# Kernel optimization log

Measured on AMD Instinct MI355X. Metric: run time of the kernel, lower is better.

## Reference

```python
import jax, jax.numpy as jnp
import numpy as np

DIM = 1024
NH = 16
HD = DIM // NH  # 64
NT = max(1, int(NH * 0.25))  # 4 time heads
NS = NH - NT                 # 12 space heads
SCALE = HD ** (-0.5)


def setup_inputs() -> dict:
    key = jax.random.key(0)
    ks = jax.random.split(key, 8)
    B, T = 2, 2048
    init = 0.02
    return {
        "x": jax.random.normal(ks[0], (B, T, DIM), dtype=jnp.float32),
        # weights stored as (in, out); torch Linear y = x @ W.T is equivalent
        "Wqt": jax.random.normal(ks[1], (DIM, NT * HD), dtype=jnp.float32) * init,
        "Wkt": jax.random.normal(ks[2], (DIM, NT * HD), dtype=jnp.float32) * init,
        "Wqs": jax.random.normal(ks[3], (DIM, NS * HD), dtype=jnp.float32) * init,
        "Wks": jax.random.normal(ks[4], (DIM, NS * HD), dtype=jnp.float32) * init,
        "Wv": jax.random.normal(ks[5], (DIM, DIM), dtype=jnp.float32) * init,
        "Wout": jax.random.normal(ks[6], (DIM, DIM), dtype=jnp.float32) * init,
        "bout": jnp.zeros((DIM,), dtype=jnp.float32),
        "w_sigma": jnp.zeros((1,), dtype=jnp.float32),
    }


def reference(x, Wqt, Wkt, Wqs, Wks, Wv, Wout, bout, w_sigma):
    B, T, D = x.shape
    Qt = (x @ Wqt).reshape(B, T, NT, HD)
    Kt = (x @ Wkt).reshape(B, T, NT, HD)
    Qs = (x @ Wqs).reshape(B, T, NS, HD)
    Ks = (x @ Wks).reshape(B, T, NS, HD)
    st = jnp.einsum('bthd,bshd->bths', Qt, Kt)  # [B,T,NT,T]
    ss = jnp.einsum('bthd,bshd->bths', Qs, Ks)  # [B,T,NS,T]
    sig = jax.nn.sigmoid(w_sigma)  # shape (1,), broadcasts
    score = jnp.concatenate([-sig * st, ss], axis=2) * SCALE  # [B,T,NH,T]
    attn = jax.nn.softmax(score, axis=-1)
    V = (x @ Wv).reshape(B, T, NH, HD)
    ctx = jnp.einsum('bths,bshd->bthd', attn, V).reshape(B, T, D)
    return ctx @ Wout + bout
```

## Files before the change

### kernel.cpp

```cpp
#include <hip/hip_runtime.h>
#include <hip/hip_bf16.h>

typedef __bf16 bf16_t;
typedef __bf16 bf16x2 __attribute__((ext_vector_type(2)));
typedef __bf16 bf16x4 __attribute__((ext_vector_type(4)));
typedef __bf16 bf16x8 __attribute__((ext_vector_type(8)));
typedef float  f32x4  __attribute__((ext_vector_type(4)));

#define DIM     1024
#define NHEAD   16
#define HDIM    64
#define NTIME   4
#define TSEQ    2048
#define NBATCH  2
#define SCALE_F 0.125f
#define LOG2E   1.4426950408889634f

#define GLL(gp, lp) __builtin_amdgcn_global_load_lds( \
    (const __attribute__((address_space(1))) unsigned int*)(const void*)(gp), \
    (__attribute__((address_space(3))) unsigned int*)(void*)(lp), 16, 0, 0)

#define OFF_WQKVT 0UL
#define OFF_WOUTT (OFF_WQKVT + 3072UL*1024UL*2UL)
#define OFF_Q     (OFF_WOUTT + 1024UL*1024UL*2UL)
#define OFF_K     (OFF_Q  + 2UL*16UL*2048UL*64UL*2UL)
#define OFF_VT    (OFF_K  + 2UL*16UL*2048UL*64UL*2UL)
#define OFF_CTX   (OFF_VT + 2UL*16UL*2048UL*64UL*2UL)

__global__ void prep_all(const float* __restrict__ x,
                         const float* __restrict__ Wqt, const float* __restrict__ Wkt,
                         const float* __restrict__ Wqs, const float* __restrict__ Wks,
                         const float* __restrict__ Wv,  const float* __restrict__ Wout,
                         bf16_t* __restrict__ Xb, bf16_t* __restrict__ WqkvT,
                         bf16_t* __restrict__ WoutT) {
    __shared__ float T[64][65];
    const int bid = blockIdx.x;
    if (bid < 2048) {
        int i = bid * 256 + threadIdx.x;
        const float4* s = (const float4*)(x + (size_t)i * 8);
        float4 a = s[0], b2 = s[1];
        bf16x8 v;
        v[0] = (bf16_t)a.x;  v[1] = (bf16_t)a.y;  v[2] = (bf16_t)a.z;  v[3] = (bf16_t)a.w;
        v[4] = (bf16_t)b2.x; v[5] = (bf16_t)b2.y; v[6] = (bf16_t)b2.z; v[7] = (bf16_t)b2.w;
        *(bf16x8*)(Xb + (size_t)i * 8) = v;
        return;
    }
    const int tc = threadIdx.x & 63, tr = threadIdx.x >> 6;
    const int sc = threadIdx.x & 31, sr = threadIdx.x >> 5;
    if (bid < 2816) {
        const int l = bid - 2048;
        const int n0 = (l % 48) * 64;
        const int k0 = (l / 48) * 64;
        const int region = n0 >> 10;
        const int cc = n0 & 1023;
        const int h = cc >> 6;
        const float* src; int ncols, col0;
        if (region == 2) { src = Wv; ncols = 1024; col0 = cc; }
        else if (h < NTIME) { src = (region == 0) ? Wqt : Wkt; ncols = NTIME * HDIM; col0 = h * HDIM; }
        else                { src = (region == 0) ? Wqs : Wks; ncols = (NHEAD - NTIME) * HDIM; col0 = (h - NTIME) * HDIM; }
#pragma unroll
        for (int i = 0; i < 16; ++i) {
            int kl = tr * 16 + i;
            T[kl][tc] = src[(size_t)(k0 + kl) * ncols + col0 + tc];
        }
        __syncthreads();
#pragma unroll
        for (int i = 0; i < 8; ++i) {
            int nl = sr * 8 + i;
            bf16x2 w;
            w[0] = (bf16_t)T[sc * 2][nl];
            w[1] = (bf16_t)T[sc * 2 + 1][nl];
            *(bf16x2*)(WqkvT + (size_t)(n0 + nl) * 1024 + k0 + sc * 2) = w;
        }
    } else {
        const int l = bid - 2816;
        const int n0 = (l % 16) * 64;
        const int k0 = (l / 16) * 64;
#pragma unroll
        for (int i = 0; i < 16; ++i) {
            int kl = tr * 16 + i;
            T[kl][tc] = Wout[(size_t)(k0 + kl) * 1024 + n0 + tc];
        }
        __syncthreads();
#pragma unroll
        for (int i = 0; i < 8; ++i) {
            int nl = sr * 8 + i;
            bf16x2 w;
            w[0] = (bf16_t)T[sc * 2][nl];
            w[1] = (bf16_t)T[sc * 2 + 1][nl];
            *(bf16x2*)(WoutT + (size_t)(n0 + nl) * 1024 + k0 + sc * 2) = w;
        }
    }
}

template<int MODE, int NB, int FN>
__global__ __launch_bounds__(256)
void gemm_bf16(const bf16_t* __restrict__ Ab, const bf16_t* __restrict__ Bt,
               bf16_t* __restrict__ Qb, bf16_t* __restrict__ Kb, bf16_t* __restrict__ Vt,
               float* __restrict__ Cout, const float* __restrict__ bias)
{
    __shared__ __align__(16) bf16_t As[3][128][32];
    __shared__ __align__(16) bf16_t Bs[3][FN * 32][32];

    constexpr int NXC = NB / 8;
    const int xcd = blockIdx.x & 7;
    const int r   = blockIdx.x >> 3;
    const int m0 = (r / NXC) * 128;
    const int n0 = (xcd * NXC + r % NXC) * (FN * 32);

    const int tid  = threadIdx.x;
    const int lane = tid & 63;
    const int wave = tid >> 6;
    const int wm = (wave >> 1) * 64, wn = (wave & 1) * (FN * 16);
    const int g = lane >> 4, lr = lane & 15;

    f32x4 acc[4][FN];
#pragma unroll
    for (int i = 0; i < 4; ++i)
#pragma unroll
        for (int j = 0; j < FN; ++j) acc[i][j] = f32x4{0.f, 0.f, 0.f, 0.f};

    auto stage = [&](int k0, int buf) {
#pragma unroll
        for (int c = 0; c < 2; ++c) {
            int idx  = tid + c * 256;
            int row  = idx >> 2;
            int csrc = (idx & 3) ^ ((row >> 1) & 3);
            GLL(Ab + (size_t)(m0 + row) * 1024 + k0 + csrc * 8,
                (char*)&As[buf][0][0] + (c * 256 + wave * 64) * 16);
            if (c < FN / 2)
                GLL(Bt + (size_t)(n0 + row) * 1024 + k0 + csrc * 8,
                    (char*)&Bs[buf][0][0] + (c * 256 + wave * 64) * 16);
        }
    };

    stage(0, 0);
    stage(32, 1);

    for (int t = 0; t < 32; ++t) {
        if (t < 31) {
            if constexpr (FN == 4) asm volatile("s_waitcnt vmcnt(4)" ::: "memory");
            else                   asm volatile("s_waitcnt vmcnt(3)" ::: "memory");
        } else {
            asm volatile("s_waitcnt vmcnt(0)" ::: "memory");
        }
        __builtin_amdgcn_s_barrier();
        __builtin_amdgcn_sched_barrier(0);
        if (t + 2 < 32) stage((t + 2) * 32, (t + 2) % 3);

        const int buf = t % 3;
        const char* Ac = (const char*)&As[buf][0][0];
        const char* Bc = (const char*)&Bs[buf][0][0];
        bf16x8 afr[4], bfr[FN];
#pragma unroll
        for (int f = 0; f < 4; ++f) {
            int ra = wm + f * 16 + lr;
            afr[f] = *(const bf16x8*)(Ac + ra * 64 + ((g ^ ((ra >> 1) & 3)) << 4));
        }
#pragma unroll
        for (int f = 0; f < FN; ++f) {
            int rb = wn + f * 16 + lr;
            bfr[f] = *(const bf16x8*)(Bc + rb * 64 + ((g ^ ((rb >> 1) & 3)) << 4));
        }
        __builtin_amdgcn_s_setprio(1);
#pragma unroll
        for (int fm = 0; fm < 4; ++fm)
#pragma unroll
            for (int fn = 0; fn < FN; ++fn)
                acc[fm][fn] = __builtin_amdgcn_mfma_f32_16x16x32_bf16(bfr[fn], afr[fm], acc[fm][fn], 0, 0, 0);
        __builtin_amdgcn_s_setprio(0);
    }

    const int region = n0 >> 10;
#pragma unroll
    for (int fm = 0; fm < 4; ++fm) {
        const int m = m0 + wm + fm * 16 + lr;
        const int b = m >> 11, t = m & 2047;
        const int ts = (t & ~31) | (((t >> 2) & 3) << 3) | (((t >> 4) & 1) << 2) | (t & 3);
#pragma unroll
        for (int fn = 0; fn < FN; ++fn) {
            const int nb = n0 + wn + fn * 16 + g * 4;
            if constexpr (MODE == 1) {
                float4 bb = *(const float4*)(bias + nb);
                float4 v;
                v.x = acc[fm][fn][0] + bb.x;
                v.y = acc[fm][fn][1] + bb.y;
                v.z = acc[fm][fn][2] + bb.z;
                v.w = acc[fm][fn][3] + bb.w;
                *(float4*)(Cout + (size_t)m * DIM + nb) = v;
            } else {
                const int cc = nb & 1023;
                const int h = cc >> 6, d0 = cc & 63;
                const size_t bh = (size_t)(b * NHEAD + h);
                if (region == 2) {
#pragma unroll
                    for (int r2 = 0; r2 < 4; ++r2)
                        Vt[(bh * HDIM + d0 + r2) * TSEQ + ts] = (bf16_t)acc[fm][fn][r2];
                } else {
                    bf16x4 w;
#pragma unroll
                    for (int r2 = 0; r2 < 4; ++r2) w[r2] = (bf16_t)acc[fm][fn][r2];
                    bf16_t* dst = (region == 0) ? Qb : Kb;
                    *(bf16x4*)(dst + (bh * TSEQ + t) * HDIM + d0) = w;
                }
            }
        }
    }
}

__global__ __launch_bounds__(256, 2)
void attn_kernel(const bf16_t* __restrict__ Qb, const bf16_t* __restrict__ Kb,
                 const bf16_t* __restrict__ Vt, bf16_t* __restrict__ ctx,
                 const float* __restrict__ w_sigma)
{
    __shared__ __align__(16) bf16_t Ktile[4][64][64];
    __shared__ __align__(16) bf16_t Vtile[4][64][64];

    const int l    = ((blockIdx.x & 7) << 6) + (blockIdx.x >> 3);
    const int qc   = l & 15;
    const int bh   = l >> 4;
    const int h    = bh & 15;
    const int b    = bh >> 4;
    const int tid  = threadIdx.x;
    const int lane = tid & 63;
    const int wave = tid >> 6;
    const int g = lane >> 4, lr = lane & 15;
    const int q0 = qc * 128 + wave * 32;

    const float sig = 1.f / (1.f + __expf(-w_sigma[0]));
    const float fl2 = ((h < NTIME) ? (-sig * SCALE_F) : SCALE_F) * LOG2E;

    const bf16_t* Qp = Qb + (size_t)bh * TSEQ * HDIM;
    const bf16_t* Kp = Kb + (size_t)bh * TSEQ * HDIM;
    const bf16_t* Vp = Vt + (size_t)bh * HDIM * TSEQ;

    bf16x8 qa0 = *(const bf16x8*)(Qp + (size_t)(q0 + lr) * HDIM + g * 8);
    bf16x8 qa1 = *(const bf16x8*)(Qp + (size_t)(q0 + lr) * HDIM + 32 + g * 8);
    bf16x8 qb0 = *(const bf16x8*)(Qp + (size_t)(q0 + 16 + lr) * HDIM + g * 8);
    bf16x8 qb1 = *(const bf16x8*)(Qp + (size_t)(q0 + 16 + lr) * HDIM + 32 + g * 8);
#pragma unroll
    for (int e = 0; e < 8; ++e) {
        qa0[e] = (bf16_t)((float)qa0[e] * fl2);
        qa1[e] = (bf16_t)((float)qa1[e] * fl2);
        qb0[e] = (bf16_t)((float)qb0[e] * fl2);
        qb1[e] = (bf16_t)((float)qb1[e] * fl2);
    }

    f32x4 oA[4], oB[4];
#pragma unroll
    for (int n = 0; n < 4; ++n) { oA[n] = f32x4{0.f,0.f,0.f,0.f}; oB[n] = f32x4{0.f,0.f,0.f,0.f}; }
    float lpA = 0.f, lpB = 0.f;

    const int trow = tid >> 3;
    const int tcg  = tid & 7;

    auto stage = [&](int s0, int buf) {
#pragma unroll
        for (int j = 0; j < 2; ++j) {
            int kr = j * 32 + trow;
            GLL(Kp + (size_t)(s0 + kr) * HDIM + ((tcg ^ (kr & 7)) << 3),
                (char*)&Ktile[buf][0][0] + (j * 256 + wave * 64) * 16);
            int vr = j * 32 + trow;
            GLL(Vp + (size_t)vr * TSEQ + s0 + ((tcg ^ (vr & 7)) << 3),
                (char*)&Vtile[buf][0][0] + (j * 256 + wave * 64) * 16);
        }
    };

    auto compute = [&](const char* Kt, const char* Vc) {
        bf16x8 paA[2], paB[2];
        __builtin_amdgcn_s_setprio(1);
#pragma unroll
        for (int st = 0; st < 4; ++st) {
            const int srow = st * 16 + lr;
            const int rs7 = lr & 7;
            bf16x8 kb0 = *(const bf16x8*)(Kt + srow * 128 + ((g ^ rs7) << 4));
            bf16x8 kb1 = *(const bf16x8*)(Kt + srow * 128 + (((4 + g) ^ rs7) << 4));
            f32x4 zA = f32x4{0.f,0.f,0.f,0.f}, zB = f32x4{0.f,0.f,0.f,0.f};
            zA = __builtin_amdgcn_mfma_f32_16x16x32_bf16(kb0, qa0, zA, 0, 0, 0);
            zA = __builtin_amdgcn_mfma_f32_16x16x32_bf16(kb1, qa1, zA, 0, 0, 0);
            zB = __builtin_amdgcn_mfma_f32_16x16x32_bf16(kb0, qb0, zB, 0, 0, 0);
            zB = __builtin_amdgcn_mfma_f32_16x16x32_bf16(kb1, qb1, zB, 0, 0, 0);
            float a0 = __builtin_amdgcn_exp2f(zA[0]);
            float a1 = __builtin_amdgcn_exp2f(zA[1]);
            float a2 = __builtin_amdgcn_exp2f(zA[2]);
            float a3 = __builtin_amdgcn_exp2f(zA[3]);
            float b0 = __builtin_amdgcn_exp2f(zB[0]);
            float b1 = __builtin_amdgcn_exp2f(zB[1]);
            float b2 = __builtin_amdgcn_exp2f(zB[2]);
            float b3 = __builtin_amdgcn_exp2f(zB[3]);
            const int kc = st >> 1, e0 = (st & 1) * 4;
            paA[kc][e0]     = (bf16_t)a0; paA[kc][e0 + 1] = (bf16_t)a1;
            paA[kc][e0 + 2] = (bf16_t)a2; paA[kc][e0 + 3] = (bf16_t)a3;
            paB[kc][e0]     = (bf16_t)b0; paB[kc][e0 + 1] = (bf16_t)b1;
            paB[kc][e0 + 2] = (bf16_t)b2; paB[kc][e0 + 3] = (bf16_t)b3;
            lpA += (a0 + a1) + (a2 + a3);
            lpB += (b0 + b1) + (b2 + b3);
        }
        __builtin_amdgcn_s_setprio(0);

        __builtin_amdgcn_s_setprio(1);
#pragma unroll
        for (int kc = 0; kc < 2; ++kc) {
#pragma unroll
            for (int n = 0; n < 4; ++n) {
                const int row = n * 16 + lr;
                bf16x8 vb = *(const bf16x8*)(Vc + row * 128 + (((kc * 4 + g) ^ (row & 7)) << 4));
                oA[n] = __builtin_amdgcn_mfma_f32_16x16x32_bf16(vb, paA[kc], oA[n], 0, 0, 0);
                oB[n] = __builtin_amdgcn_mfma_f32_16x16x32_bf16(vb, paB[kc], oB[n], 0, 0, 0);
            }
        }
        __builtin_amdgcn_s_setprio(0);
    };

    stage(0, 0);
    stage(64, 1);

    for (int step = 0; step < 32; ++step) {
        if (step + 2 < 32) stage((step + 2) * 64, (step + 2) & 3);
        if (step < 30)       asm volatile("s_waitcnt vmcnt(8)" ::: "memory");
        else if (step == 30) asm volatile("s_waitcnt vmcnt(4)" ::: "memory");
        else                 asm volatile("s_waitcnt vmcnt(0)" ::: "memory");
        __builtin_amdgcn_s_barrier();
        __builtin_amdgcn_sched_barrier(0);
        const int buf = step & 3;
        compute((const char*)&Ktile[buf][0][0], (const char*)&Vtile[buf][0][0]);
    }

    float lfA = lpA, lfB = lpB;
    lfA += __shfl_xor(lfA, 16, 64);
    lfA += __shfl_xor(lfA, 32, 64);
    lfB += __shfl_xor(lfB, 16, 64);
    lfB += __shfl_xor(lfB, 32, 64);
    float liA = 1.f / lfA, liB = 1.f / lfB;

    const int tA = q0 + lr, tB = q0 + 16 + lr;
#pragma unroll
    for (int n = 0; n < 4; ++n) {
        bf16x4 wA, wB;
#pragma unroll
        for (int r = 0; r < 4; ++r) {
            wA[r] = (bf16_t)(oA[n][r] * liA);
            wB[r] = (bf16_t)(oB[n][r] * liB);
        }
        *(bf16x4*)(ctx + ((size_t)(b * TSEQ + tA)) * DIM + h * HDIM + n * 16 + g * 4) = wA;
        *(bf16x4*)(ctx + ((size_t)(b * TSEQ + tB)) * DIM + h * HDIM + n * 16 + g * 4) = wB;
    }
}

extern "C" void kernel_launch(void* const* d_in, const int* in_sizes, int n_in,
                              void* d_out, int out_size, void* d_ws, size_t ws_size,
                              hipStream_t stream) {
    const float* x    = (const float*)d_in[0];
    const float* Wqt  = (const float*)d_in[1];
    const float* Wkt  = (const float*)d_in[2];
    const float* Wqs  = (const float*)d_in[3];
    const float* Wks  = (const float*)d_in[4];
    const float* Wv   = (const float*)d_in[5];
    const float* Wout = (const float*)d_in[6];
    const float* bout = (const float*)d_in[7];
    const float* wsig = (const float*)d_in[8];
    (void)in_sizes; (void)n_in; (void)out_size; (void)ws_size;

    char* ws = (char*)d_ws;
    bf16_t* WqkvT = (bf16_t*)(ws + OFF_WQKVT);
    bf16_t* WoutT = (bf16_t*)(ws + OFF_WOUTT);
    bf16_t* Qb    = (bf16_t*)(ws + OFF_Q);
    bf16_t* Kb    = (bf16_t*)(ws + OFF_K);
    bf16_t* Vt    = (bf16_t*)(ws + OFF_VT);
    bf16_t* ctx   = (bf16_t*)(ws + OFF_CTX);
    bf16_t* Xb    = ctx;
    float*  out   = (float*)d_out;

    prep_all<<<3072, 256, 0, stream>>>(x, Wqt, Wkt, Wqs, Wks, Wv, Wout, Xb, WqkvT, WoutT);

    gemm_bf16<0, 24, 4><<<768, 256, 0, stream>>>(Xb, WqkvT, Qb, Kb, Vt, nullptr, nullptr);

    attn_kernel<<<512, 256, 0, stream>>>(Qb, Kb, Vt, ctx, wsig);

    gemm_bf16<1, 16, 2><<<512, 256, 0, stream>>>(ctx, WoutT, nullptr, nullptr, nullptr, out, bout);
}
```

Baseline: 108.6 us.

## Replace QKV projection GEMM with 256x256-tile 8-wave double-buffered kernel

Adds a dedicated QKV projection kernel with 256x256 output tiles, 512 threads, K-step 64, XOR-swizzled LDS and double buffering, replacing the 128x128 triple-buffered generic GEMM. The larger tiles raise arithmetic intensity and cut global/LDS traffic per MFMA. The kernel interleaves the next tile's prefetch with the first phase of fragment loads. The cost is fewer blocks (192 on a 256-CU part, below one wave of CUs), full vmcnt(0) waits each step, and extra barriers per phase, which may leave CUs idle. The generic GEMM is simplified to its output-projection mode only.

```diff
diff --git a/kernel.cpp b/kernel.cpp
--- a/kernel.cpp
+++ b/kernel.cpp
@@ -93,10 +93,125 @@
     }
 }
 
-template<int MODE, int NB, int FN>
+__global__ __launch_bounds__(512, 2)
+void gemm1_8ph(const bf16_t* __restrict__ Ab, const bf16_t* __restrict__ Bt,
+               bf16_t* __restrict__ Qb, bf16_t* __restrict__ Kb, bf16_t* __restrict__ Vt)
+{
+    __shared__ __align__(16) bf16_t As[2][256][64];
+    __shared__ __align__(16) bf16_t Bs[2][256][64];
+
+    const int l  = (blockIdx.x & 7) * 24 + (blockIdx.x >> 3);
+    const int m0 = (l / 12) * 256;
+    const int n0 = (l % 12) * 256;
+
+    const int tid  = threadIdx.x;
+    const int lane = tid & 63;
+    const int wave = tid >> 6;
+    const int wm = (wave >> 2) * 128;
+    const int wn = (wave & 3) * 64;
+    const int g = lane >> 4, lr = lane & 15;
+
+    f32x4 acc[8][4];
+#pragma unroll
+    for (int i = 0; i < 8; ++i)
+#pragma unroll
+        for (int j = 0; j < 4; ++j) acc[i][j] = f32x4{0.f, 0.f, 0.f, 0.f};
+
+    const int srow = tid >> 3;
+    const int scg  = tid & 7;
+
+    auto stageTile = [&](int k0, int buf) {
+#pragma unroll
+        for (int hf = 0; hf < 2; ++hf) {
+#pragma unroll
+            for (int j = 0; j < 2; ++j) {
+                int row = hf * 128 + j * 64 + srow;
+                GLL(Ab + (size_t)(m0 + row) * 1024 + k0 + ((scg ^ (row & 7)) << 3),
+                    (char*)&As[buf][0][0] + hf * 16384 + j * 8192 + wave * 1024);
+                GLL(Bt + (size_t)(n0 + row) * 1024 + k0 + ((scg ^ (row & 7)) << 3),
+                    (char*)&Bs[buf][0][0] + hf * 16384 + j * 8192 + wave * 1024);
+            }
+        }
+    };
+
+    stageTile(0, 0);
+
+    for (int t = 0; t < 16; ++t) {
+        const int cur = t & 1;
+        asm volatile("s_waitcnt vmcnt(0)" ::: "memory");
+        __builtin_amdgcn_s_barrier();
+        __builtin_amdgcn_sched_barrier(0);
+
+        const char* Ac = (const char*)&As[cur][0][0];
+        const char* Bc = (const char*)&Bs[cur][0][0];
+
+        bf16x8 bfr[4][2];
+#pragma unroll
+        for (int p = 0; p < 4; ++p) {
+            if (p == 0) {
+                if (t + 1 < 16) stageTile((t + 1) * 64, cur ^ 1);
+#pragma unroll
+                for (int n = 0; n < 4; ++n) {
+                    int rb = wn + n * 16 + lr;
+#pragma unroll
+                    for (int kk = 0; kk < 2; ++kk)
+                        bfr[n][kk] = *(const bf16x8*)(Bc + rb * 128 + (((kk * 4 + g) ^ (rb & 7)) << 4));
+                }
+            }
+            bf16x8 afr[2][2];
+#pragma unroll
+            for (int d = 0; d < 2; ++d) {
+                int ra = wm + (2 * p + d) * 16 + lr;
+#pragma unroll
+                for (int kk = 0; kk < 2; ++kk)
+                    afr[d][kk] = *(const bf16x8*)(Ac + ra * 128 + (((kk * 4 + g) ^ (ra & 7)) << 4));
+            }
+            asm volatile("s_waitcnt lgkmcnt(0)" ::: "memory");
+            __builtin_amdgcn_sched_barrier(0);
+            __builtin_amdgcn_s_setprio(1);
+#pragma unroll
+            for (int d = 0; d < 2; ++d)
+#pragma unroll
+                for (int kk = 0; kk < 2; ++kk)
+#pragma unroll
+                    for (int n = 0; n < 4; ++n)
+                        acc[2 * p + d][n] = __builtin_amdgcn_mfma_f32_16x16x32_bf16(
+                            bfr[n][kk], afr[d][kk], acc[2 * p + d][n], 0, 0, 0);
+            __builtin_amdgcn_s_setprio(0);
+            __builtin_amdgcn_s_barrier();
+        }
+    }
+
+    const int region = n0 >> 10;
+#pragma unroll
+    for (int fm = 0; fm < 8; ++fm) {
+        const int m = m0 + wm + fm * 16 + lr;
+        const int b = m >> 11, tt = m & 2047;
+        const int ts = (tt & ~31) | (((tt >> 2) & 3) << 3) | (((tt >> 4) & 1) << 2) | (tt & 3);
+#pragma unroll
+        for (int fn = 0; fn < 4; ++fn) {
+            const int nb = n0 + wn + fn * 16 + g * 4;
+            const int cc = nb & 1023;
+            const int h = cc >> 6, d0 = cc & 63;
+            const size_t bh = (size_t)(b * NHEAD + h);
+            if (region == 2) {
+#pragma unroll
+                for (int r2 = 0; r2 < 4; ++r2)
+                    Vt[(bh * HDIM + d0 + r2) * TSEQ + ts] = (bf16_t)acc[fm][fn][r2];
+            } else {
+                bf16x4 w;
+#pragma unroll
+                for (int r2 = 0; r2 < 4; ++r2) w[r2] = (bf16_t)acc[fm][fn][r2];
+                bf16_t* dst = (region == 0) ? Qb : Kb;
+                *(bf16x4*)(dst + (bh * TSEQ + tt) * HDIM + d0) = w;
+            }
+        }
+    }
+}
+
+template<int NB, int FN>
 __global__ __launch_bounds__(256)
 void gemm_bf16(const bf16_t* __restrict__ Ab, const bf16_t* __restrict__ Bt,
-               bf16_t* __restrict__ Qb, bf16_t* __restrict__ Kb, bf16_t* __restrict__ Vt,
                float* __restrict__ Cout, const float* __restrict__ bias)
 {
     __shared__ __align__(16) bf16_t As[3][128][32];
@@ -138,12 +253,8 @@
     stage(32, 1);
 
     for (int t = 0; t < 32; ++t) {
-        if (t < 31) {
-            if constexpr (FN == 4) asm volatile("s_waitcnt vmcnt(4)" ::: "memory");
-            else                   asm volatile("s_waitcnt vmcnt(3)" ::: "memory");
-        } else {
-            asm volatile("s_waitcnt vmcnt(0)" ::: "memory");
-        }
+        if (t < 31) asm volatile("s_waitcnt vmcnt(3)" ::: "memory");
+        else        asm volatile("s_waitcnt vmcnt(0)" ::: "memory");
         __builtin_amdgcn_s_barrier();
         __builtin_amdgcn_sched_barrier(0);
         if (t + 2 < 32) stage((t + 2) * 32, (t + 2) % 3);
@@ -171,39 +282,19 @@
         __builtin_amdgcn_s_setprio(0);
     }
 
-    const int region = n0 >> 10;
 #pragma unroll
     for (int fm = 0; fm < 4; ++fm) {
         const int m = m0 + wm + fm * 16 + lr;
-        const int b = m >> 11, t = m & 2047;
-        const int ts = (t & ~31) | (((t >> 2) & 3) << 3) | (((t >> 4) & 1) << 2) | (t & 3);
 #pragma unroll
         for (int fn = 0; fn < FN; ++fn) {
             const int nb = n0 + wn + fn * 16 + g * 4;
-            if constexpr (MODE == 1) {
-                float4 bb = *(const float4*)(bias + nb);
-                float4 v;
-                v.x = acc[fm][fn][0] + bb.x;
-                v.y = acc[fm][fn][1] + bb.y;
-                v.z = acc[fm][fn][2] + bb.z;
-                v.w = acc[fm][fn][3] + bb.w;
-                *(float4*)(Cout + (size_t)m * DIM + nb) = v;
-            } else {
-                const int cc = nb & 1023;
-                const int h = cc >> 6, d0 = cc & 63;
-                const size_t bh = (size_t)(b * NHEAD + h);
-                if (region == 2) {
-#pragma unroll
-                    for (int r2 = 0; r2 < 4; ++r2)
-                        Vt[(bh * HDIM + d0 + r2) * TSEQ + ts] = (bf16_t)acc[fm][fn][r2];
-                } else {
-                    bf16x4 w;
-#pragma unroll
-                    for (int r2 = 0; r2 < 4; ++r2) w[r2] = (bf16_t)acc[fm][fn][r2];
-                    bf16_t* dst = (region == 0) ? Qb : Kb;
-                    *(bf16x4*)(dst + (bh * TSEQ + t) * HDIM + d0) = w;
-                }
-            }
+            float4 bb = *(const float4*)(bias + nb);
+            float4 v;
+            v.x = acc[fm][fn][0] + bb.x;
+            v.y = acc[fm][fn][1] + bb.y;
+            v.z = acc[fm][fn][2] + bb.z;
+            v.w = acc[fm][fn][3] + bb.w;
+            *(float4*)(Cout + (size_t)m * DIM + nb) = v;
         }
     }
 }
@@ -373,9 +464,9 @@
 
     prep_all<<<3072, 256, 0, stream>>>(x, Wqt, Wkt, Wqs, Wks, Wv, Wout, Xb, WqkvT, WoutT);
 
-    gemm_bf16<0, 24, 4><<<768, 256, 0, stream>>>(Xb, WqkvT, Qb, Kb, Vt, nullptr, nullptr);
+    gemm1_8ph<<<192, 512, 0, stream>>>(Xb, WqkvT, Qb, Kb, Vt);
 
     attn_kernel<<<512, 256, 0, stream>>>(Qb, Kb, Vt, ctx, wsig);
 
-    gemm_bf16<1, 16, 2><<<512, 256, 0, stream>>>(ctx, WoutT, nullptr, nullptr, nullptr, out, bout);
+    gemm_bf16<16, 2><<<512, 256, 0, stream>>>(ctx, WoutT, out, bout);
 }
```

Result: slower. 115.0 us (+5.9%).
